# Kernel optimization log

Measured on AMD Instinct MI355X. Metric: run time of the kernel, lower is better.

Reference implementation:

```python
import jax, jax.numpy as jnp
import numpy as np

N, E, D = 50000, 800000, 64


def setup_inputs() -> dict:
    key = jax.random.key(0)
    ks = jax.random.split(key, 24)
    s = 1.0 / np.sqrt(D)
    inp = {
        'x': jax.random.normal(ks[0], (N, D), dtype=jnp.float32),
        'edge_index': jax.random.randint(ks[1], (2, E), 0, N, dtype=jnp.int32),
        'edge_attr_emb': jax.random.normal(ks[2], (E, D), dtype=jnp.float32),
    }
    names = ['Wq1', 'Wk1', 'Wv1', 'We1', 'Ws1', 'Wq2', 'Wk2', 'Wv2', 'We2', 'Ws2']
    for i, n in enumerate(names):
        inp[n] = jax.random.normal(ks[3 + i], (D, D), dtype=jnp.float32) * s
    for n in ['bq1', 'bk1', 'bv1', 'bs1', 'bq2', 'bk2', 'bv2', 'bs2']:
        inp[n] = jnp.zeros((D,), dtype=jnp.float32)
    return inp


def transformer_conv(x, src, dst, ea, Wq, bq, Wk, bk, Wv, bv, We, Ws, bs):
    # PyG TransformerConv, heads=1, concat=True, beta=False, root_weight=True
    q = x @ Wq + bq                      # [N, D]
    k = x @ Wk + bk                      # [N, D]
    v = x @ Wv + bv                      # [N, D]
    e = ea @ We                          # [E, D] (lin_edge has no bias)
    k_e = k[src] + e                     # gather source keys, modulate by edge
    logits = jnp.sum(q[dst] * k_e, axis=-1) / jnp.sqrt(jnp.asarray(D, x.dtype))  # [E]
    m = jax.ops.segment_max(logits, dst, num_segments=N)   # per-target max
    a = jnp.exp(logits - m[dst])
    denom = jax.ops.segment_sum(a, dst, num_segments=N)
    alpha = a / denom[dst]               # segment softmax over incoming edges
    msg = (v[src] + e) * alpha[:, None]  # [E, D]
    out = jax.ops.segment_sum(msg, dst, num_segments=N)    # scatter-add
    return out + x @ Ws + bs             # root/skip connection


def reference(x, edge_index, edge_attr_emb,
              Wq1, bq1, Wk1, bk1, Wv1, bv1, We1, Ws1, bs1,
              Wq2, bq2, Wk2, bk2, Wv2, bv2, We2, Ws2, bs2):
    src, dst = edge_index[0], edge_index[1]
    r = jax.nn.relu(x)
    r = transformer_conv(r, src, dst, edge_attr_emb, Wq1, bq1, Wk1, bk1, Wv1, bv1, We1, Ws1, bs1)
    r = jax.nn.relu(r)
    r = transformer_conv(r, src, dst, edge_attr_emb, Wq2, bq2, Wk2, bk2, Wv2, bv2, We2, Ws2, bs2)
    return x + r  # identity residual since l_in == l_out
```

## Files before the change

### kernel.cpp

```cpp
#include <hip/hip_runtime.h>

#define NN 50000
#define EE 800000
#define SCAN_B 196

__global__ __launch_bounds__(256) void k_hist(const int* __restrict__ ei,
                                              int* __restrict__ deg) {
    int i = blockIdx.x * 256 + threadIdx.x;
    if (i < EE) atomicAdd(&deg[ei[EE + i]], 1);
}

__global__ __launch_bounds__(256) void k_scanA(const int* __restrict__ deg,
                                               int* __restrict__ loc,
                                               int* __restrict__ bsum) {
    __shared__ int sh[256];
    int t = threadIdx.x, i = blockIdx.x * 256 + t;
    int v = (i < NN) ? deg[i] : 0;
    sh[t] = v;
    __syncthreads();
    for (int off = 1; off < 256; off <<= 1) {
        int u = (t >= off) ? sh[t - off] : 0;
        __syncthreads();
        sh[t] += u;
        __syncthreads();
    }
    if (i < NN) loc[i] = sh[t] - v;
    if (t == 255) bsum[blockIdx.x] = sh[255];
}

__global__ __launch_bounds__(256) void k_scanB(const int* __restrict__ bsum,
                                               int* __restrict__ boff) {
    __shared__ int sh[256];
    int t = threadIdx.x;
    int v = (t < SCAN_B) ? bsum[t] : 0;
    sh[t] = v;
    __syncthreads();
    for (int off = 1; off < 256; off <<= 1) {
        int u = (t >= off) ? sh[t - off] : 0;
        __syncthreads();
        sh[t] += u;
        __syncthreads();
    }
    if (t < SCAN_B) boff[t] = sh[t] - v;
}

__global__ __launch_bounds__(256) void k_scanC(const int* __restrict__ loc,
                                               const int* __restrict__ boff,
                                               int* __restrict__ rowptr,
                                               int* __restrict__ cursor) {
    int t = threadIdx.x, i = blockIdx.x * 256 + t;
    if (i < NN) {
        int r = loc[i] + boff[blockIdx.x];
        rowptr[i] = r;
        cursor[i] = r;
    }
    if (i == 0) rowptr[NN] = EE;
}

__global__ __launch_bounds__(256) void k_fill(const int* __restrict__ ei,
                                              int* __restrict__ cursor,
                                              int* __restrict__ esrc,
                                              int* __restrict__ eidx) {
    int i = blockIdx.x * 256 + threadIdx.x;
    if (i < EE) {
        int d = ei[EE + i];
        int pos = atomicAdd(&cursor[d], 1);
        esrc[pos] = ei[i];
        eidx[pos] = i;
    }
}

__global__ __launch_bounds__(64) void fuse_weights(
    const float* __restrict__ Wq, const float* __restrict__ We,
    const float* __restrict__ bq, float* __restrict__ Wqe,
    float* __restrict__ bqe) {
    int j = threadIdx.x;
    int t = blockIdx.x;
    if (t < 64) {
        float acc = 0.f;
        #pragma unroll
        for (int d = 0; d < 64; ++d) acc = fmaf(Wq[t * 64 + d], We[j * 64 + d], acc);
        Wqe[t * 64 + j] = acc;
    } else {
        float acc = 0.f;
        #pragma unroll
        for (int d = 0; d < 64; ++d) acc = fmaf(bq[d], We[j * 64 + d], acc);
        bqe[j] = acc;
    }
}

__global__ __launch_bounds__(256) void node_linear(
    const float* __restrict__ hin,
    const float* __restrict__ Wq, const float* __restrict__ Wk,
    const float* __restrict__ Wv, const float* __restrict__ Wsk,
    const float* __restrict__ Wqe,
    const float* __restrict__ bq, const float* __restrict__ bk,
    const float* __restrict__ bv, const float* __restrict__ bs,
    const float* __restrict__ bqe,
    float* __restrict__ q, float* __restrict__ k, float* __restrict__ v,
    float* __restrict__ skip, float* __restrict__ qe) {
    __shared__ float r[4][64];
    int wid = threadIdx.x >> 6, lane = threadIdx.x & 63;
    int n = blockIdx.x * 4 + wid;
    float xv = hin[n * 64 + lane];
    r[wid][lane] = xv > 0.f ? xv : 0.f;
    __syncthreads();
    float aq = 0.f, ak = 0.f, av = 0.f, as_ = 0.f, aqe = 0.f;
    #pragma unroll 8
    for (int j = 0; j < 64; ++j) {
        float rj = r[wid][j];
        aq  = fmaf(rj, Wq [j * 64 + lane], aq);
        ak  = fmaf(rj, Wk [j * 64 + lane], ak);
        av  = fmaf(rj, Wv [j * 64 + lane], av);
        as_ = fmaf(rj, Wsk[j * 64 + lane], as_);
        aqe = fmaf(rj, Wqe[j * 64 + lane], aqe);
    }
    int o = n * 64 + lane;
    q[o]    = aq  + bq[lane];
    k[o]    = ak  + bk[lane];
    v[o]    = av  + bv[lane];
    skip[o] = as_ + bs[lane];
    qe[o]   = aqe + bqe[lane];
}

__global__ __launch_bounds__(256) void node_attn(
    const int* __restrict__ rowptr, const int* __restrict__ esrc,
    const int* __restrict__ eidx,
    const float* __restrict__ ea, const float* __restrict__ q,
    const float* __restrict__ k, const float* __restrict__ v,
    const float* __restrict__ qe, const float* __restrict__ skip,
    const float* __restrict__ We, const float* __restrict__ addx,
    float* __restrict__ out) {
    __shared__ float sh[4][64];
    int wid = threadIdx.x >> 6, lane = threadIdx.x & 63;
    int n = blockIdx.x * 4 + wid;
    int beg = rowptr[n], end = rowptr[n + 1];
    size_t no = (size_t)n * 64 + lane;
    float qd = q[no], qed = qe[no];
    float m = -3.0e38f, den = 0.f, av = 0.f, ae = 0.f;

    float kv_n = 0.f, vv_n = 0.f, eav_n = 0.f;
    if (beg < end) {
        int s0 = esrc[beg], e0 = eidx[beg];
        kv_n  = k[(size_t)s0 * 64 + lane];
        vv_n  = v[(size_t)s0 * 64 + lane];
        eav_n = ea[(size_t)e0 * 64 + lane];
    }
    for (int p = beg; p < end; ++p) {
        float kv = kv_n, vv = vv_n, eav = eav_n;
        if (p + 1 < end) {
            int s2 = esrc[p + 1], e2 = eidx[p + 1];
            kv_n  = k[(size_t)s2 * 64 + lane];
            vv_n  = v[(size_t)s2 * 64 + lane];
            eav_n = ea[(size_t)e2 * 64 + lane];
        }
        float t = fmaf(qd, kv, qed * eav);
        #pragma unroll
        for (int off = 32; off; off >>= 1) t += __shfl_xor(t, off);
        float lg = t * 0.125f;
        if (lg > m) {
            float sc = __expf(m - lg);
            den *= sc; av *= sc; ae *= sc; m = lg;
        }
        float a = __expf(lg - m);
        den += a;
        av = fmaf(a, vv, av);
        ae = fmaf(a, eav, ae);
    }
    sh[wid][lane] = ae;
    __syncthreads();
    float r = 0.f;
    #pragma unroll 8
    for (int j = 0; j < 64; ++j) r = fmaf(sh[wid][j], We[j * 64 + lane], r);
    float o = (den > 0.f) ? (av + r) / den : 0.f;
    o += skip[no];
    if (addx) o += addx[no];
    out[no] = o;
}

extern "C" void kernel_launch(void* const* d_in, const int* in_sizes, int n_in,
                              void* d_out, int out_size, void* d_ws, size_t ws_size,
                              hipStream_t stream) {
    const float* x  = (const float*)d_in[0];
    const int*   ei = (const int*)d_in[1];
    const float* ea = (const float*)d_in[2];
    const float* W[10];
    for (int i = 0; i < 10; ++i) W[i] = (const float*)d_in[3 + i];
    const float* B[8];
    for (int i = 0; i < 8; ++i) B[i] = (const float*)d_in[13 + i];

    const size_t ND = (size_t)NN * 64;
    float* ws   = (float*)d_ws;
    float* q    = ws;
    float* k    = ws + 1 * ND;
    float* v    = ws + 2 * ND;
    float* skip = ws + 3 * ND;
    float* qe   = ws + 4 * ND;
    float* h    = ws + 5 * ND;
    int* deg    = (int*)(ws + 6 * ND);
    int* loc    = deg + NN;
    int* bsum   = loc + NN;
    int* boff   = bsum + 256;
    int* rowptr = boff + 256;
    int* cursor = rowptr + NN + 1;
    int* esrc   = cursor + NN;
    int* eidx   = esrc + EE;
    float* Wqe  = (float*)(eidx + EE);
    float* bqe  = Wqe + 4096;

    (void)hipMemsetAsync(deg, 0, NN * sizeof(int), stream);
    k_hist <<<(EE + 255) / 256, 256, 0, stream>>>(ei, deg);
    k_scanA<<<SCAN_B, 256, 0, stream>>>(deg, loc, bsum);
    k_scanB<<<1, 256, 0, stream>>>(bsum, boff);
    k_scanC<<<SCAN_B, 256, 0, stream>>>(loc, boff, rowptr, cursor);
    k_fill <<<(EE + 255) / 256, 256, 0, stream>>>(ei, cursor, esrc, eidx);

    for (int l = 0; l < 2; ++l) {
        const float* Wq = W[l * 5 + 0], *Wk = W[l * 5 + 1], *Wv = W[l * 5 + 2];
        const float* We = W[l * 5 + 3], *Wsk = W[l * 5 + 4];
        const float* bq = B[l * 4 + 0], *bk = B[l * 4 + 1];
        const float* bv = B[l * 4 + 2], *bs = B[l * 4 + 3];

        fuse_weights<<<65, 64, 0, stream>>>(Wq, We, bq, Wqe, bqe);
        node_linear<<<NN / 4, 256, 0, stream>>>(
            l ? h : x, Wq, Wk, Wv, Wsk, Wqe, bq, bk, bv, bs, bqe,
            q, k, v, skip, qe);
        node_attn<<<NN / 4, 256, 0, stream>>>(
            rowptr, esrc, eidx, ea, q, k, v, qe, skip, We,
            l ? x : nullptr, l ? (float*)d_out : h);
    }
}
```

Baseline: 1.013 ms.

## Process four edges per wavefront with float4 lanes and packed edge indices

The attention kernel now splits each 64-lane wavefront into four 16-lane groups. Each group handles a different incoming edge and loads its k, v and edge-attribute rows as float4. The online softmax max is shared across the groups, and the groups' partial sums are combined with shuffles before the edge-weight projection. Source and edge indices are also packed into a single int2 array. The aim is fewer serial loop iterations, fewer shuffle reductions per edge and wider memory transactions, at the cost of idle lanes in the last partial batch for nodes with low degree.

```diff
diff --git a/kernel.cpp b/kernel.cpp
--- a/kernel.cpp
+++ b/kernel.cpp
@@ -1,4 +1,5 @@
 #include <hip/hip_runtime.h>
+#include <math.h>
 
 #define NN 50000
 #define EE 800000
@@ -59,14 +60,12 @@
 
 __global__ __launch_bounds__(256) void k_fill(const int* __restrict__ ei,
                                               int* __restrict__ cursor,
-                                              int* __restrict__ esrc,
-                                              int* __restrict__ eidx) {
+                                              int2* __restrict__ es) {
     int i = blockIdx.x * 256 + threadIdx.x;
     if (i < EE) {
         int d = ei[EE + i];
         int pos = atomicAdd(&cursor[d], 1);
-        esrc[pos] = ei[i];
-        eidx[pos] = i;
+        es[pos] = make_int2(ei[i], i);
     }
 }
 
@@ -123,56 +122,101 @@
     qe[o]   = aqe + bqe[lane];
 }
 
+__device__ __forceinline__ float dot4(float4 a, float4 b) {
+    return fmaf(a.x, b.x, fmaf(a.y, b.y, fmaf(a.z, b.z, a.w * b.w)));
+}
+__device__ __forceinline__ float4 f4scale(float4 a, float s) {
+    return make_float4(a.x * s, a.y * s, a.z * s, a.w * s);
+}
+__device__ __forceinline__ float4 f4fma(float s, float4 a, float4 acc) {
+    return make_float4(fmaf(s, a.x, acc.x), fmaf(s, a.y, acc.y),
+                       fmaf(s, a.z, acc.z), fmaf(s, a.w, acc.w));
+}
+__device__ __forceinline__ float4 f4shflxor_add(float4 a, int mask) {
+    a.x += __shfl_xor(a.x, mask);
+    a.y += __shfl_xor(a.y, mask);
+    a.z += __shfl_xor(a.z, mask);
+    a.w += __shfl_xor(a.w, mask);
+    return a;
+}
+
 __global__ __launch_bounds__(256) void node_attn(
-    const int* __restrict__ rowptr, const int* __restrict__ esrc,
-    const int* __restrict__ eidx,
+    const int* __restrict__ rowptr, const int2* __restrict__ es,
     const float* __restrict__ ea, const float* __restrict__ q,
     const float* __restrict__ k, const float* __restrict__ v,
     const float* __restrict__ qe, const float* __restrict__ skip,
     const float* __restrict__ We, const float* __restrict__ addx,
     float* __restrict__ out) {
-    __shared__ float sh[4][64];
+    __shared__ float shA[4][64];
+    __shared__ float shE[4][64];
     int wid = threadIdx.x >> 6, lane = threadIdx.x & 63;
+    int g = lane >> 4, li = lane & 15;
     int n = blockIdx.x * 4 + wid;
     int beg = rowptr[n], end = rowptr[n + 1];
-    size_t no = (size_t)n * 64 + lane;
-    float qd = q[no], qed = qe[no];
-    float m = -3.0e38f, den = 0.f, av = 0.f, ae = 0.f;
-
-    float kv_n = 0.f, vv_n = 0.f, eav_n = 0.f;
+
+    const float4* q4  = (const float4*)q;
+    const float4* qe4 = (const float4*)qe;
+    const float4* k4  = (const float4*)k;
+    const float4* v4  = (const float4*)v;
+    const float4* ea4 = (const float4*)ea;
+
+    float4 qd  = q4 [(size_t)n * 16 + li];
+    float4 qed = qe4[(size_t)n * 16 + li];
+
+    float m = -3.0e38f, den = 0.f;
+    float4 av = make_float4(0, 0, 0, 0), ae = make_float4(0, 0, 0, 0);
+
     if (beg < end) {
-        int s0 = esrc[beg], e0 = eidx[beg];
-        kv_n  = k[(size_t)s0 * 64 + lane];
-        vv_n  = v[(size_t)s0 * 64 + lane];
-        eav_n = ea[(size_t)e0 * 64 + lane];
-    }
-    for (int p = beg; p < end; ++p) {
-        float kv = kv_n, vv = vv_n, eav = eav_n;
-        if (p + 1 < end) {
-            int s2 = esrc[p + 1], e2 = eidx[p + 1];
-            kv_n  = k[(size_t)s2 * 64 + lane];
-            vv_n  = v[(size_t)s2 * 64 + lane];
-            eav_n = ea[(size_t)e2 * 64 + lane];
+        bool vldc; float4 kvc, vvc, evc;
+        {
+            int idx = beg + g; vldc = idx < end; int ci = vldc ? idx : beg;
+            int2 se = es[ci];
+            kvc = k4[(size_t)se.x * 16 + li];
+            vvc = v4[(size_t)se.x * 16 + li];
+            evc = ea4[(size_t)se.y * 16 + li];
         }
-        float t = fmaf(qd, kv, qed * eav);
-        #pragma unroll
-        for (int off = 32; off; off >>= 1) t += __shfl_xor(t, off);
-        float lg = t * 0.125f;
-        if (lg > m) {
-            float sc = __expf(m - lg);
-            den *= sc; av *= sc; ae *= sc; m = lg;
+        for (int p = beg; p < end; p += 4) {
+            bool vldn = false; float4 kvn, vvn, evn;
+            if (p + 4 < end) {
+                int idx = p + 4 + g; vldn = idx < end; int ci = vldn ? idx : beg;
+                int2 se = es[ci];
+                kvn = k4[(size_t)se.x * 16 + li];
+                vvn = v4[(size_t)se.x * 16 + li];
+                evn = ea4[(size_t)se.y * 16 + li];
+            }
+            float t = dot4(qd, kvc) + dot4(qed, evc);
+            t += __shfl_xor(t, 1);
+            t += __shfl_xor(t, 2);
+            t += __shfl_xor(t, 4);
+            t += __shfl_xor(t, 8);
+            float lg = vldc ? t * 0.125f : -INFINITY;
+            float mx = fmaxf(lg, __shfl_xor(lg, 16));
+            mx = fmaxf(mx, __shfl_xor(mx, 32));
+            if (mx > m) {
+                float sc = __expf(m - mx);
+                den *= sc; av = f4scale(av, sc); ae = f4scale(ae, sc);
+                m = mx;
+            }
+            float a = __expf(lg - m);
+            den += a;
+            av = f4fma(a, vvc, av);
+            ae = f4fma(a, evc, ae);
+            vldc = vldn; kvc = kvn; vvc = vvn; evc = evn;
         }
-        float a = __expf(lg - m);
-        den += a;
-        av = fmaf(a, vv, av);
-        ae = fmaf(a, eav, ae);
-    }
-    sh[wid][lane] = ae;
+    }
+    av = f4shflxor_add(av, 16); av = f4shflxor_add(av, 32);
+    ae = f4shflxor_add(ae, 16); ae = f4shflxor_add(ae, 32);
+    den += __shfl_xor(den, 16); den += __shfl_xor(den, 32);
+    if (lane < 16) {
+        *(float4*)&shA[wid][lane * 4] = av;
+        *(float4*)&shE[wid][lane * 4] = ae;
+    }
     __syncthreads();
     float r = 0.f;
     #pragma unroll 8
-    for (int j = 0; j < 64; ++j) r = fmaf(sh[wid][j], We[j * 64 + lane], r);
-    float o = (den > 0.f) ? (av + r) / den : 0.f;
+    for (int j = 0; j < 64; ++j) r = fmaf(shE[wid][j], We[j * 64 + lane], r);
+    size_t no = (size_t)n * 64 + lane;
+    float o = (den > 0.f) ? (shA[wid][lane] + r) / den : 0.f;
     o += skip[no];
     if (addx) o += addx[no];
     out[no] = o;
@@ -203,9 +247,8 @@
     int* boff   = bsum + 256;
     int* rowptr = boff + 256;
     int* cursor = rowptr + NN + 1;
-    int* esrc   = cursor + NN;
-    int* eidx   = esrc + EE;
-    float* Wqe  = (float*)(eidx + EE);
+    int2* es    = (int2*)(cursor + NN + 1);
+    float* Wqe  = (float*)(es + EE);
     float* bqe  = Wqe + 4096;
 
     (void)hipMemsetAsync(deg, 0, NN * sizeof(int), stream);
@@ -213,7 +256,7 @@
     k_scanA<<<SCAN_B, 256, 0, stream>>>(deg, loc, bsum);
     k_scanB<<<1, 256, 0, stream>>>(bsum, boff);
     k_scanC<<<SCAN_B, 256, 0, stream>>>(loc, boff, rowptr, cursor);
-    k_fill <<<(EE + 255) / 256, 256, 0, stream>>>(ei, cursor, esrc, eidx);
+    k_fill <<<(EE + 255) / 256, 256, 0, stream>>>(ei, cursor, es);
 
     for (int l = 0; l < 2; ++l) {
         const float* Wq = W[l * 5 + 0], *Wk = W[l * 5 + 1], *Wv = W[l * 5 + 2];
@@ -226,7 +269,7 @@
             l ? h : x, Wq, Wk, Wv, Wsk, Wqe, bq, bk, bv, bs, bqe,
             q, k, v, skip, qe);
         node_attn<<<NN / 4, 256, 0, stream>>>(
-            rowptr, esrc, eidx, ea, q, k, v, qe, skip, We,
+            rowptr, es, ea, q, k, v, qe, skip, We,
             l ? x : nullptr, l ? (float*)d_out : h);
     }
 }
```

After: 898.1 us. 1.13x faster.
